# Performance work log

Hardware: AMD Instinct MI355X
Metric: run time of the kernel (lower is better)

The kernel has to match this reference:

```python
import jax, jax.numpy as jnp
import numpy as np

BN_EPS = 1e-5


def setup_inputs() -> dict:
    key = jax.random.key(0)
    ks = jax.random.split(key, 8)
    B, S, D = 2048, 64, 128      # batch, seq_len, d_in
    H, DK = 8, 16                # n_head, d_k; H*DK == 128
    F = H * DK
    std = np.sqrt(2.0 / DK).astype(np.float32)
    return {
        "v": jax.random.normal(ks[0], (B, S, D), jnp.float32),
        "Wq": jax.random.normal(ks[1], (F, D), jnp.float32) * std,
        "bq": jnp.zeros((F,), jnp.float32),
        "bn_gamma": jnp.ones((F,), jnp.float32),
        "bn_beta": jnp.zeros((F,), jnp.float32),
        "W2": jax.random.normal(ks[2], (F, F), jnp.float32) * (1.0 / np.sqrt(F)),
        "b2": jnp.zeros((F,), jnp.float32),
        "Wk": jax.random.normal(ks[3], (F, D), jnp.float32) * std,
        "bk": jnp.zeros((F,), jnp.float32),
    }


def reference(v, Wq, bq, bn_gamma, bn_beta, W2, b2, Wk, bk):
    # v: [B, S, D]
    B, S, D = v.shape
    F = Wq.shape[0]
    H = 8
    DK = F // H
    temperature = jnp.asarray(np.sqrt(DK), v.dtype)

    # q path: linear -> mean over seq -> BatchNorm1d (batch stats) -> linear
    q = jnp.einsum("bsd,fd->bsf", v, Wq) + bq          # [B, S, F]
    q = q.mean(axis=1)                                  # [B, F]
    mu = q.mean(axis=0)
    var = q.var(axis=0)                                 # biased, as BN uses
    q = (q - mu) * jax.lax.rsqrt(var + BN_EPS) * bn_gamma + bn_beta
    q = jnp.einsum("bf,gf->bg", q, W2) + b2             # [B, F]
    q = q.reshape(B, H, DK).transpose(1, 0, 2)          # [H, B, DK]

    # k path
    k = (jnp.einsum("bsd,fd->bsf", v, Wk) + bk).reshape(B, S, H, DK)
    k = k.transpose(2, 0, 1, 3)                         # [H, B, S, DK]

    # single query per (head, batch): scores over seq
    attn = jnp.einsum("hbd,hbsd->hbs", q, k) / temperature
    attn = jax.nn.softmax(attn, axis=-1)                # [H, B, S]
    # dropout is identity in eval mode

    # weighted sum over seq of the ORIGINAL v (torch repeats v per head;
    # broadcasting avoids materializing the repeat)
    out = jnp.einsum("hbs,bsd->hbd", attn, v)           # [H, B, D]
    return out, attn
```

## Files before the change

kernel.cpp:

```cpp
#include <hip/hip_runtime.h>

#define B_ 2048
#define S_ 64
#define D_ 128
#define F_ 128
#define H_ 8

__global__ __launch_bounds__(256) void k_q1(const float* __restrict__ v,
                                            const float* __restrict__ Wq,
                                            const float* __restrict__ bq,
                                            float* __restrict__ q1,
                                            float* __restrict__ gsum) {
  const int b = blockIdx.x;
  const int t = threadIdx.x;
  if (b == 0) gsum[t] = 0.f;

  __shared__ float red[8 * 128];
  __shared__ __align__(16) float vbarL[128];

  const int c4 = t & 31;
  const int r0 = t >> 5;
  const float4* v4 = (const float4*)(v + (size_t)b * (S_ * D_));
  float4 acc = {0.f, 0.f, 0.f, 0.f};
  #pragma unroll
  for (int i = 0; i < 8; ++i) {
    float4 x = v4[(r0 * 8 + i) * 32 + c4];
    acc.x += x.x; acc.y += x.y; acc.z += x.z; acc.w += x.w;
  }
  red[r0 * 128 + c4 * 4 + 0] = acc.x;
  red[r0 * 128 + c4 * 4 + 1] = acc.y;
  red[r0 * 128 + c4 * 4 + 2] = acc.z;
  red[r0 * 128 + c4 * 4 + 3] = acc.w;
  __syncthreads();
  if (t < 128) {
    float s = 0.f;
    #pragma unroll
    for (int r = 0; r < 8; ++r) s += red[r * 128 + t];
    vbarL[t] = s * (1.0f / 64.0f);
  }
  __syncthreads();

  const float4* Wq4 = (const float4*)Wq;
  const float4* vb4 = (const float4*)vbarL;
  const int d4 = t & 31;
  const int fg = t >> 5;
  #pragma unroll
  for (int fi = 0; fi < 16; ++fi) {
    int f = fi * 8 + fg;
    float4 w = Wq4[f * 32 + d4];
    float4 vv = vb4[d4];
    float p = w.x * vv.x + w.y * vv.y + w.z * vv.z + w.w * vv.w;
    #pragma unroll
    for (int off = 16; off; off >>= 1) p += __shfl_down(p, off, 32);
    if (d4 == 0) q1[b * F_ + f] = p + bq[f];
  }
}

__global__ __launch_bounds__(256) void k_stats2(const float* __restrict__ q1,
                                                const float* __restrict__ W2,
                                                float* __restrict__ gsum,
                                                float* __restrict__ gsq,
                                                float* __restrict__ W2t) {
  const int blk = blockIdx.x;
  const int t = threadIdx.x;
  const int f4 = t & 31, rg = t >> 5;
  const int r0 = blk * 32;
  const float4* q14 = (const float4*)q1;
  float4 s = {0.f, 0.f, 0.f, 0.f};
  float4 q = {0.f, 0.f, 0.f, 0.f};
  #pragma unroll
  for (int k = 0; k < 4; ++k) {
    float4 x = q14[(size_t)(r0 + rg + 8 * k) * 32 + f4];
    s.x += x.x; s.y += x.y; s.z += x.z; s.w += x.w;
    q.x += x.x * x.x; q.y += x.y * x.y; q.z += x.z * x.z; q.w += x.w * x.w;
  }
  __shared__ float rs[8][128], rq[8][128];
  rs[rg][f4 * 4 + 0] = s.x; rs[rg][f4 * 4 + 1] = s.y;
  rs[rg][f4 * 4 + 2] = s.z; rs[rg][f4 * 4 + 3] = s.w;
  rq[rg][f4 * 4 + 0] = q.x; rq[rg][f4 * 4 + 1] = q.y;
  rq[rg][f4 * 4 + 2] = q.z; rq[rg][f4 * 4 + 3] = q.w;
  __syncthreads();
  if (t < 128) {
    float ss = 0.f, qq = 0.f;
    #pragma unroll
    for (int r = 0; r < 8; ++r) { ss += rs[r][t]; qq += rq[r][t]; }
    atomicAdd(&gsum[t], ss);
    atomicAdd(&gsq[t], qq);
  }
  {
    int g = blk * 2 + (t >> 7);
    int f = t & 127;
    W2t[f * 128 + g] = W2[g * 128 + f];
  }
}

__global__ __launch_bounds__(64) void k_mid(const float* __restrict__ q1,
                                            const float* __restrict__ gsum,
                                            const float* __restrict__ gsq,
                                            const float* __restrict__ gamma,
                                            const float* __restrict__ beta,
                                            const float* __restrict__ W2t,
                                            const float* __restrict__ b2,
                                            const float* __restrict__ Wk,
                                            const float* __restrict__ bk,
                                            float* __restrict__ qW,
                                            float* __restrict__ qb) {
  const int b = blockIdx.x;
  const int lane = threadIdx.x;
  __shared__ __align__(16) float qnL[128];
  __shared__ __align__(16) float q2L[128];

  #pragma unroll
  for (int j = 0; j < 2; ++j) {
    int f = lane + j * 64;
    float mu = gsum[f] * (1.0f / (float)B_);
    float var = gsq[f] * (1.0f / (float)B_) - mu * mu;
    float rsg = rsqrtf(var + 1e-5f) * gamma[f];
    qnL[f] = q1[(size_t)b * F_ + f] * rsg + (beta[f] - mu * rsg);
  }
  __syncthreads();

  {
    const int g4 = lane & 31, fh = lane >> 5;
    const float4* W2t4 = (const float4*)W2t;
    float4 acc = {0.f, 0.f, 0.f, 0.f};
    #pragma unroll 8
    for (int f = fh; f < 128; f += 2) {
      float qv = qnL[f];
      float4 w = W2t4[f * 32 + g4];
      acc.x += qv * w.x; acc.y += qv * w.y; acc.z += qv * w.z; acc.w += qv * w.w;
    }
    acc.x += __shfl_xor(acc.x, 32, 64);
    acc.y += __shfl_xor(acc.y, 32, 64);
    acc.z += __shfl_xor(acc.z, 32, 64);
    acc.w += __shfl_xor(acc.w, 32, 64);
    if (fh == 0) {
      float4 bb = ((const float4*)b2)[g4];
      acc.x += bb.x; acc.y += bb.y; acc.z += bb.z; acc.w += bb.w;
      ((float4*)q2L)[g4] = acc;
    }
  }
  __syncthreads();

  {
    const int d4 = lane & 31, hh = lane >> 5;
    const float4* Wk4 = (const float4*)Wk;
    #pragma unroll
    for (int k = 0; k < 4; ++k) {
      int h = k * 2 + hh;
      float4 acc = {0.f, 0.f, 0.f, 0.f};
      const float* q2row = &q2L[h * 16];
      #pragma unroll
      for (int dk = 0; dk < 16; ++dk) {
        float qv = q2row[dk];
        float4 w = Wk4[(h * 16 + dk) * 32 + d4];
        acc.x += qv * w.x; acc.y += qv * w.y; acc.z += qv * w.z; acc.w += qv * w.w;
      }
      ((float4*)qW)[(size_t)b * 256 + h * 32 + d4] = acc;
    }
  }
  if (lane < 8) {
    float acc = 0.f;
    #pragma unroll
    for (int dk = 0; dk < 16; ++dk)
      acc += q2L[lane * 16 + dk] * bk[lane * 16 + dk];
    qb[b * 8 + lane] = acc;
  }
}

__global__ __launch_bounds__(256) void k_attn(const float* __restrict__ v,
                                              const float* __restrict__ qW,
                                              const float* __restrict__ qb,
                                              float* __restrict__ outp) {
  const int b = blockIdx.x;
  const int t = threadIdx.x;
  __shared__ __align__(16) float vL[64 * 128];
  __shared__ __align__(16) float qWL[8 * 128];
  __shared__ float attnL[8 * 64];
  __shared__ float qbL[8];

  float4* vL4 = (float4*)vL;
  const float4* vg4 = (const float4*)(v + (size_t)b * (S_ * D_));
  #pragma unroll
  for (int i = 0; i < 8; ++i) {
    int idx = i * 256 + t;
    int s = idx >> 5, c4 = idx & 31;
    vL4[s * 32 + (c4 ^ (s & 31))] = vg4[idx];
  }
  {
    const float4* qWg4 = (const float4*)(qW + (size_t)b * (H_ * D_));
    ((float4*)qWL)[t] = qWg4[t];
  }
  if (t < 8) qbL[t] = qb[b * 8 + t];
  __syncthreads();

  const int s = t & 63;
  const int hq = t >> 6;
  const int h0 = hq * 2, h1 = hq * 2 + 1;
  const float4* qWL4 = (const float4*)qWL;
  float a0 = 0.f, a1 = 0.f;
  #pragma unroll
  for (int d4 = 0; d4 < 32; ++d4) {
    float4 vv = vL4[s * 32 + (d4 ^ (s & 31))];
    float4 w0 = qWL4[h0 * 32 + d4];
    float4 w1 = qWL4[h1 * 32 + d4];
    a0 += vv.x * w0.x + vv.y * w0.y + vv.z * w0.z + vv.w * w0.w;
    a1 += vv.x * w1.x + vv.y * w1.y + vv.z * w1.z + vv.w * w1.w;
  }
  float l0 = (a0 + qbL[h0]) * 0.25f;
  float l1 = (a1 + qbL[h1]) * 0.25f;

  float m0 = l0, m1 = l1;
  #pragma unroll
  for (int off = 32; off; off >>= 1) {
    m0 = fmaxf(m0, __shfl_xor(m0, off, 64));
    m1 = fmaxf(m1, __shfl_xor(m1, off, 64));
  }
  float e0 = __expf(l0 - m0), e1 = __expf(l1 - m1);
  float s0 = e0, s1 = e1;
  #pragma unroll
  for (int off = 32; off; off >>= 1) {
    s0 += __shfl_xor(s0, off, 64);
    s1 += __shfl_xor(s1, off, 64);
  }
  float at0 = e0 / s0, at1 = e1 / s1;
  attnL[h0 * 64 + s] = at0;
  attnL[h1 * 64 + s] = at1;
  float* attn_out = outp + (size_t)H_ * B_ * D_;
  attn_out[(size_t)h0 * (B_ * S_) + b * S_ + s] = at0;
  attn_out[(size_t)h1 * (B_ * S_) + b * S_ + s] = at1;
  __syncthreads();

  const int d4o = t & 31;
  const int h = t >> 5;
  float4 acc = {0.f, 0.f, 0.f, 0.f};
  #pragma unroll
  for (int si = 0; si < 64; ++si) {
    float a = attnL[h * 64 + si];
    float4 vv = vL4[si * 32 + (d4o ^ (si & 31))];
    acc.x += a * vv.x; acc.y += a * vv.y; acc.z += a * vv.z; acc.w += a * vv.w;
  }
  ((float4*)outp)[(size_t)h * (B_ * 32) + b * 32 + d4o] = acc;
}

extern "C" void kernel_launch(void* const* d_in, const int* in_sizes, int n_in,
                              void* d_out, int out_size, void* d_ws, size_t ws_size,
                              hipStream_t stream) {
  const float* v     = (const float*)d_in[0];
  const float* Wq    = (const float*)d_in[1];
  const float* bq    = (const float*)d_in[2];
  const float* gamma = (const float*)d_in[3];
  const float* beta  = (const float*)d_in[4];
  const float* W2    = (const float*)d_in[5];
  const float* b2    = (const float*)d_in[6];
  const float* Wk    = (const float*)d_in[7];
  const float* bk    = (const float*)d_in[8];

  float* ws = (float*)d_ws;
  float* q1v  = ws;
  float* gsum = q1v + (size_t)B_ * F_;
  float* gsq  = gsum + 128;
  float* W2t  = gsq + 128;
  float* qWv  = W2t + 128 * 128;
  float* qbv  = qWv + (size_t)B_ * H_ * D_;
  float* outp = (float*)d_out;

  hipLaunchKernelGGL(k_q1,     dim3(B_), dim3(256), 0, stream, v, Wq, bq, q1v, gsum);
  hipLaunchKernelGGL(k_stats2, dim3(64), dim3(256), 0, stream, q1v, W2, gsum, gsq, W2t);
  hipLaunchKernelGGL(k_mid,    dim3(B_), dim3(64),  0, stream, q1v, gsum, gsq,
                     gamma, beta, W2t, b2, Wk, bk, qWv, qbv);
  hipLaunchKernelGGL(k_attn,   dim3(B_), dim3(256), 0, stream, v, qWv, qbv, outp);
}
```

Baseline: 61.44 us.

## Fuse BN-normalize and q projection into attention kernel, drop k_mid launch

The per-batch normalization, W2 projection and Wk folding that k_mid did are moved into the first wave of k_attn. That wave computes them while the v tile is being staged into LDS, and the qW/qb intermediates go straight to shared memory instead of a global round trip. This removes one kernel launch and about 8 MB of global writes and reads. In exchange, the other three waves of each 256-thread block sit idle until the single-wave q computation finishes. The code relies on in-wave s_waitcnt plus a sched_barrier for LDS ordering instead of __syncthreads.

```diff
diff --git a/kernel.cpp b/kernel.cpp
--- a/kernel.cpp
+++ b/kernel.cpp
@@ -94,104 +94,96 @@
   }
 }
 
-__global__ __launch_bounds__(64) void k_mid(const float* __restrict__ q1,
-                                            const float* __restrict__ gsum,
-                                            const float* __restrict__ gsq,
-                                            const float* __restrict__ gamma,
-                                            const float* __restrict__ beta,
-                                            const float* __restrict__ W2t,
-                                            const float* __restrict__ b2,
-                                            const float* __restrict__ Wk,
-                                            const float* __restrict__ bk,
-                                            float* __restrict__ qW,
-                                            float* __restrict__ qb) {
-  const int b = blockIdx.x;
-  const int lane = threadIdx.x;
-  __shared__ __align__(16) float qnL[128];
-  __shared__ __align__(16) float q2L[128];
-
-  #pragma unroll
-  for (int j = 0; j < 2; ++j) {
-    int f = lane + j * 64;
-    float mu = gsum[f] * (1.0f / (float)B_);
-    float var = gsq[f] * (1.0f / (float)B_) - mu * mu;
-    float rsg = rsqrtf(var + 1e-5f) * gamma[f];
-    qnL[f] = q1[(size_t)b * F_ + f] * rsg + (beta[f] - mu * rsg);
-  }
-  __syncthreads();
-
-  {
-    const int g4 = lane & 31, fh = lane >> 5;
-    const float4* W2t4 = (const float4*)W2t;
-    float4 acc = {0.f, 0.f, 0.f, 0.f};
-    #pragma unroll 8
-    for (int f = fh; f < 128; f += 2) {
-      float qv = qnL[f];
-      float4 w = W2t4[f * 32 + g4];
-      acc.x += qv * w.x; acc.y += qv * w.y; acc.z += qv * w.z; acc.w += qv * w.w;
-    }
-    acc.x += __shfl_xor(acc.x, 32, 64);
-    acc.y += __shfl_xor(acc.y, 32, 64);
-    acc.z += __shfl_xor(acc.z, 32, 64);
-    acc.w += __shfl_xor(acc.w, 32, 64);
-    if (fh == 0) {
-      float4 bb = ((const float4*)b2)[g4];
-      acc.x += bb.x; acc.y += bb.y; acc.z += bb.z; acc.w += bb.w;
-      ((float4*)q2L)[g4] = acc;
-    }
-  }
-  __syncthreads();
-
-  {
-    const int d4 = lane & 31, hh = lane >> 5;
-    const float4* Wk4 = (const float4*)Wk;
-    #pragma unroll
-    for (int k = 0; k < 4; ++k) {
-      int h = k * 2 + hh;
-      float4 acc = {0.f, 0.f, 0.f, 0.f};
-      const float* q2row = &q2L[h * 16];
-      #pragma unroll
-      for (int dk = 0; dk < 16; ++dk) {
-        float qv = q2row[dk];
-        float4 w = Wk4[(h * 16 + dk) * 32 + d4];
-        acc.x += qv * w.x; acc.y += qv * w.y; acc.z += qv * w.z; acc.w += qv * w.w;
-      }
-      ((float4*)qW)[(size_t)b * 256 + h * 32 + d4] = acc;
-    }
-  }
-  if (lane < 8) {
-    float acc = 0.f;
-    #pragma unroll
-    for (int dk = 0; dk < 16; ++dk)
-      acc += q2L[lane * 16 + dk] * bk[lane * 16 + dk];
-    qb[b * 8 + lane] = acc;
-  }
-}
-
 __global__ __launch_bounds__(256) void k_attn(const float* __restrict__ v,
-                                              const float* __restrict__ qW,
-                                              const float* __restrict__ qb,
+                                              const float* __restrict__ q1,
+                                              const float* __restrict__ gsum,
+                                              const float* __restrict__ gsq,
+                                              const float* __restrict__ gamma,
+                                              const float* __restrict__ beta,
+                                              const float* __restrict__ W2t,
+                                              const float* __restrict__ b2,
+                                              const float* __restrict__ Wk,
+                                              const float* __restrict__ bk,
                                               float* __restrict__ outp) {
   const int b = blockIdx.x;
   const int t = threadIdx.x;
   __shared__ __align__(16) float vL[64 * 128];
   __shared__ __align__(16) float qWL[8 * 128];
+  __shared__ __align__(16) float qnL[128];
+  __shared__ __align__(16) float q2L[128];
   __shared__ float attnL[8 * 64];
   __shared__ float qbL[8];
 
   float4* vL4 = (float4*)vL;
   const float4* vg4 = (const float4*)(v + (size_t)b * (S_ * D_));
   #pragma unroll
-  for (int i = 0; i < 8; ++i) {
-    int idx = i * 256 + t;
-    int s = idx >> 5, c4 = idx & 31;
-    vL4[s * 32 + (c4 ^ (s & 31))] = vg4[idx];
-  }
-  {
-    const float4* qWg4 = (const float4*)(qW + (size_t)b * (H_ * D_));
-    ((float4*)qWL)[t] = qWg4[t];
-  }
-  if (t < 8) qbL[t] = qb[b * 8 + t];
+  for (int j = 0; j < 8; ++j) {
+    int idx = j * 256 + t;
+    int s = idx >> 5, cc = idx & 31;
+    vL4[s * 32 + (cc ^ (s & 31))] = vg4[idx];
+  }
+
+  if (t < 64) {
+    const int lane = t;
+    #pragma unroll
+    for (int j = 0; j < 2; ++j) {
+      int f = lane + j * 64;
+      float mu = gsum[f] * (1.0f / (float)B_);
+      float var = gsq[f] * (1.0f / (float)B_) - mu * mu;
+      float rsg = rsqrtf(var + 1e-5f) * gamma[f];
+      qnL[f] = q1[(size_t)b * F_ + f] * rsg + (beta[f] - mu * rsg);
+    }
+    asm volatile("s_waitcnt lgkmcnt(0)" ::: "memory");
+    __builtin_amdgcn_sched_barrier(0);
+
+    {
+      const int g4 = lane & 31, fh = lane >> 5;
+      const float4* W2t4 = (const float4*)W2t;
+      float4 acc = {0.f, 0.f, 0.f, 0.f};
+      #pragma unroll 8
+      for (int f = fh; f < 128; f += 2) {
+        float qv = qnL[f];
+        float4 w = W2t4[f * 32 + g4];
+        acc.x += qv * w.x; acc.y += qv * w.y; acc.z += qv * w.z; acc.w += qv * w.w;
+      }
+      acc.x += __shfl_xor(acc.x, 32, 64);
+      acc.y += __shfl_xor(acc.y, 32, 64);
+      acc.z += __shfl_xor(acc.z, 32, 64);
+      acc.w += __shfl_xor(acc.w, 32, 64);
+      if (fh == 0) {
+        float4 bb = ((const float4*)b2)[g4];
+        acc.x += bb.x; acc.y += bb.y; acc.z += bb.z; acc.w += bb.w;
+        ((float4*)q2L)[g4] = acc;
+      }
+    }
+    asm volatile("s_waitcnt lgkmcnt(0)" ::: "memory");
+    __builtin_amdgcn_sched_barrier(0);
+
+    {
+      const int d4 = lane & 31, hh = lane >> 5;
+      const float4* Wk4 = (const float4*)Wk;
+      #pragma unroll
+      for (int k = 0; k < 4; ++k) {
+        int h = k * 2 + hh;
+        float4 acc = {0.f, 0.f, 0.f, 0.f};
+        const float* q2row = &q2L[h * 16];
+        #pragma unroll
+        for (int dk = 0; dk < 16; ++dk) {
+          float qv = q2row[dk];
+          float4 w = Wk4[(h * 16 + dk) * 32 + d4];
+          acc.x += qv * w.x; acc.y += qv * w.y; acc.z += qv * w.z; acc.w += qv * w.w;
+        }
+        ((float4*)qWL)[h * 32 + d4] = acc;
+      }
+    }
+    if (lane < 8) {
+      float acc = 0.f;
+      #pragma unroll
+      for (int dk = 0; dk < 16; ++dk)
+        acc += q2L[lane * 16 + dk] * bk[lane * 16 + dk];
+      qbL[lane] = acc;
+    }
+  }
   __syncthreads();
 
   const int s = t & 63;
@@ -261,13 +253,10 @@
   float* gsum = q1v + (size_t)B_ * F_;
   float* gsq  = gsum + 128;
   float* W2t  = gsq + 128;
-  float* qWv  = W2t + 128 * 128;
-  float* qbv  = qWv + (size_t)B_ * H_ * D_;
   float* outp = (float*)d_out;
 
   hipLaunchKernelGGL(k_q1,     dim3(B_), dim3(256), 0, stream, v, Wq, bq, q1v, gsum);
   hipLaunchKernelGGL(k_stats2, dim3(64), dim3(256), 0, stream, q1v, W2, gsum, gsq, W2t);
-  hipLaunchKernelGGL(k_mid,    dim3(B_), dim3(64),  0, stream, q1v, gsum, gsq,
-                     gamma, beta, W2t, b2, Wk, bk, qWv, qbv);
-  hipLaunchKernelGGL(k_attn,   dim3(B_), dim3(256), 0, stream, v, qWv, qbv, outp);
-}
+  hipLaunchKernelGGL(k_attn,   dim3(B_), dim3(256), 0, stream, v, q1v, gsum, gsq,
+                     gamma, beta, W2t, b2, Wk, bk, outp);
+}
```

Result: slower. 63.82 us (+3.9%).
